# Performance work log

Measured on AMD Instinct MI355X. Metric: run time of the kernel, lower is better.

## Reference

```python
import jax, jax.numpy as jnp
import numpy as np

EMBED = 1024
ATTN = 1024
HEADS = 16
HEAD_DIM = ATTN // HEADS


def setup_inputs() -> dict:
    key = jax.random.key(0)
    ks = jax.random.split(key, 8)
    s = 1.0 / np.sqrt(EMBED)
    sa = 1.0 / np.sqrt(ATTN)
    return {
        "queries": jax.random.normal(ks[0], (4, 512, EMBED), jnp.float32),
        "context": jax.random.normal(ks[1], (4, 2048, EMBED), jnp.float32),
        "Wq": jax.random.normal(ks[2], (EMBED, ATTN), jnp.float32) * s,
        "bq": jnp.zeros((ATTN,), jnp.float32),
        "Wkv": jax.random.normal(ks[3], (EMBED, 2 * ATTN), jnp.float32) * s,
        "bkv": jnp.zeros((2 * ATTN,), jnp.float32),
        "Wo": jax.random.normal(ks[4], (ATTN, EMBED), jnp.float32) * sa,
        "bo": jnp.zeros((EMBED,), jnp.float32),
    }


def reference(queries, context, Wq, bq, Wkv, bkv, Wo, bo):
    B, Lq, _ = queries.shape
    Lk = context.shape[1]
    q = queries @ Wq + bq                      # [B, Lq, ATTN]
    kv = context @ Wkv + bkv                   # [B, Lk, 2*ATTN]
    k, v = jnp.split(kv, 2, axis=-1)
    q = q.reshape(B, Lq, HEADS, HEAD_DIM)
    k = k.reshape(B, Lk, HEADS, HEAD_DIM)
    v = v.reshape(B, Lk, HEADS, HEAD_DIM)
    scale = 1.0 / np.sqrt(HEAD_DIM)
    scores = jnp.einsum("bqhd,bkhd->bhqk", q, k) * scale
    attn = jax.nn.softmax(scores, axis=-1)
    x = jnp.einsum("bhqk,bkhd->bqhd", attn, v).reshape(B, Lq, ATTN)
    return x @ Wo + bo
```

## Files before the change

### kernel.cpp

```cpp
#include <hip/hip_runtime.h>
#include <hip/hip_bf16.h>
#include <stdint.h>

typedef unsigned short u16;
typedef __attribute__((ext_vector_type(8))) __bf16 bf16x8;
typedef __attribute__((ext_vector_type(2))) __bf16 bf16x2;
typedef __attribute__((ext_vector_type(4))) float f32x4;
typedef __attribute__((ext_vector_type(4))) u16 u16x4;
typedef __attribute__((ext_vector_type(4))) float f32x4v;

typedef __attribute__((address_space(1))) void gvoid_t;
typedef __attribute__((address_space(3))) void lvoid_t;

#define BAR()    asm volatile("s_barrier" ::: "memory")
#define WAITV0() asm volatile("s_waitcnt vmcnt(0)" ::: "memory")
#define WAITV2() asm volatile("s_waitcnt vmcnt(2)" ::: "memory")
#define WAITV4() asm volatile("s_waitcnt vmcnt(4)" ::: "memory")
#define WAITV8() asm volatile("s_waitcnt vmcnt(8)" ::: "memory")

__device__ inline u16 f2bf(float f) {
    uint32_t u = __float_as_uint(f);
    u += 0x7fff + ((u >> 16) & 1);
    return (u16)(u >> 16);
}

__device__ inline float bf2f(u16 v) {
    return __uint_as_float(((uint32_t)v) << 16);
}

__device__ inline void gll16(const void* g, void* l) {
    __builtin_amdgcn_global_load_lds((gvoid_t*)g, (lvoid_t*)l, 16, 0, 0);
}

__device__ inline f32x4 mfma16(bf16x8 a, bf16x8 b, f32x4 c) {
    return __builtin_amdgcn_mfma_f32_16x16x32_bf16(a, b, c, 0, 0, 0);
}

__device__ inline int vslot(int r) {
    int n = r >> 4;
    return ((n >> 1) << 5) + (((r >> 2) & 3) << 3) + ((n & 1) << 2) + (r & 3);
}

__global__ __launch_bounds__(256) void prep_kernel(
        const float* __restrict__ q, const float* __restrict__ c,
        const float* __restrict__ Wq, const float* __restrict__ Wkv,
        const float* __restrict__ Wo, u16* __restrict__ qb,
        u16* __restrict__ cb, u16* __restrict__ WqT,
        u16* __restrict__ WkvT, u16* __restrict__ WoT) {
    const int bid = blockIdx.x;
    const int tid = threadIdx.x;
    if (bid < 10240) {
        int i = bid * 256 + tid;
        const float* src; u16* dst; int j;
        if (i < 524288) { src = q; dst = qb; j = i; }
        else            { src = c; dst = cb; j = i - 524288; }
        f32x4v f = ((const f32x4v*)src)[j];
        u16x4 o;
        o[0] = f2bf(f[0]); o[1] = f2bf(f[1]); o[2] = f2bf(f[2]); o[3] = f2bf(f[3]);
        ((u16x4*)dst)[j] = o;
        return;
    }
    int b2 = bid - 10240;
    const float* W; u16* WT; int N, n0, k0;
    if (b2 < 1024)      { W = Wq;  WT = WqT;  N = 1024; n0 = (b2 & 31) * 32; k0 = (b2 >> 5) * 32; }
    else if (b2 < 3072) { int b3 = b2 - 1024; W = Wkv; WT = WkvT; N = 2048; n0 = (b3 & 63) * 32; k0 = (b3 >> 6) * 32; }
    else                { int b3 = b2 - 3072; W = Wo;  WT = WoT;  N = 1024; n0 = (b3 & 31) * 32; k0 = (b3 >> 5) * 32; }
    __shared__ float t[32][33];
    int x = tid & 31, y = tid >> 5;
    for (int yy = y; yy < 32; yy += 8)
        t[yy][x] = W[(size_t)(k0 + yy) * N + n0 + x];
    __syncthreads();
    for (int yy = y; yy < 32; yy += 8)
        WT[(size_t)(n0 + yy) * 1024 + k0 + x] = f2bf(t[x][yy]);
}

template <int MODE>
__global__ __launch_bounds__(512, 2) void gemm_bt(
        const u16* __restrict__ A, const u16* __restrict__ Bt,
        const float* __restrict__ bias, int M, int N, int K,
        float scale, void* __restrict__ out0) {
    __shared__ u16 lds[4][6144];
    const int NT = K >> 5;
    const int tid = threadIdx.x;
    const int lane = tid & 63, wv = tid >> 6;
    const int c16 = lane & 15, g = lane >> 4;
    const int m0 = blockIdx.y * 64, n0 = blockIdx.x * 128;

    const int idxA = (wv & 3) * 64 + lane;
    const int rA = idxA >> 2, ccA = (idxA & 3) ^ ((rA >> 1) & 3);
    const size_t offA = (size_t)(m0 + rA) * K + ccA * 8;
    const int dstA = (wv & 3) * 512;
    const int idxB = wv * 64 + lane;
    const int rB = idxB >> 2, ccB = (idxB & 3) ^ ((rB >> 1) & 3);
    const size_t offB = (size_t)(n0 + rB) * K + ccB * 8;
    const int dstB = 2048 + wv * 512;

    auto stage = [&](int t) {
        gll16(A + offA + t * 32, &lds[t & 3][dstA]);
        gll16(Bt + offB + t * 32, &lds[t & 3][dstB]);
    };

    const int wm = (wv >> 1) * 16, wn = (wv & 1) * 64;
    f32x4 acc[4] = {};

    auto compute = [&](int slot) {
        const u16* la = &lds[slot][0];
        const u16* lb = &lds[slot][2048];
        int rowa = wm + c16;
        bf16x8 af = *(const bf16x8*)&la[rowa * 32 + (g ^ ((rowa >> 1) & 3)) * 8];
        bf16x8 bfr[4];
#pragma unroll
        for (int n = 0; n < 4; n++) {
            int row = wn + n * 16 + c16;
            bfr[n] = *(const bf16x8*)&lb[row * 32 + (g ^ ((row >> 1) & 3)) * 8];
        }
#pragma unroll
        for (int n = 0; n < 4; n++)
            acc[n] = mfma16(af, bfr[n], acc[n]);
    };

    stage(0); stage(1); stage(2);

    for (int t = 0; t < NT - 2; ++t) {
        WAITV4();
        BAR();
        if (t + 3 < NT) stage(t + 3);
        compute(t & 3);
    }
    WAITV2(); BAR(); compute((NT - 2) & 3);
    WAITV0(); BAR(); compute((NT - 1) & 3);

#pragma unroll
    for (int n = 0; n < 4; n++) {
        int col = n0 + wn + n * 16 + c16;
        float bv = bias[col];
        int rowb = m0 + wm + g * 4;
#pragma unroll
        for (int j = 0; j < 4; j++) {
            float v = (acc[n][j] + bv) * scale;
            int row = rowb + j;
            if (MODE == 0) {
                ((u16*)out0)[(size_t)row * N + col] = f2bf(v);
            } else {
                ((float*)out0)[(size_t)row * N + col] = v;
            }
        }
    }
}

__global__ __launch_bounds__(512, 2) void gemm_kv_ring(
        const u16* __restrict__ A, const u16* __restrict__ Bt,
        const float* __restrict__ bias, u16* __restrict__ Kp,
        u16* __restrict__ VpT) {
    __shared__ u16 lds[4][2][256 * 32];
    const int K = 1024, NT = 32;
    const int tid = threadIdx.x;
    const int lane = tid & 63, wv = tid >> 6;
    const int c16 = lane & 15, g = lane >> 4;

    const int nwg = gridDim.x * gridDim.y;
    const int bid = blockIdx.y * gridDim.x + blockIdx.x;
    const int cpx = nwg >> 3;
    const int sw = (bid & 7) * cpx + (bid >> 3);
    const int bx = sw % gridDim.x, by = sw / gridDim.x;
    const int m0 = by * 256, n0 = bx * 256;

    const int isB = wv >> 2;
    const int rbase = (wv & 3) * 64;
    const u16* src = isB ? Bt : A;
    const int base0 = isB ? n0 : m0;
    size_t off[4];
    const u16* ldst[4];
#pragma unroll
    for (int i = 0; i < 4; i++) {
        int rl = rbase + i * 16 + (lane >> 2);
        int ch = (lane & 3) ^ ((rl >> 1) & 3);
        off[i] = (size_t)(base0 + rl) * K + ch * 8;
        ldst[i] = &lds[0][0][0] + ((size_t)isB * 256 * 32) + (size_t)(rbase + i * 16) * 32;
    }
    const size_t slotStride = 2 * 256 * 32;

    auto stage = [&](int t) {
        const u16* s0 = src + (size_t)t * 32;
        u16* d = (u16*)ldst[0] + (size_t)(t & 3) * slotStride;
        gll16(s0 + off[0], d);
        gll16(s0 + off[1], d + 16 * 32);
        gll16(s0 + off[2], d + 32 * 32);
        gll16(s0 + off[3], d + 48 * 32);
    };

    const int wm = wv >> 2;
    const int wn = wv & 3;
    f32x4 acc[8][4] = {};

    auto compute = [&](int slot) {
        const u16* la = &lds[slot][0][0];
        const u16* lb = &lds[slot][1][0];
        bf16x8 af[8], bfr[4];
#pragma unroll
        for (int m = 0; m < 8; m++) {
            int row = wm * 128 + m * 16 + c16;
            af[m] = *(const bf16x8*)&la[row * 32 + (g ^ ((row >> 1) & 3)) * 8];
        }
#pragma unroll
        for (int n = 0; n < 4; n++) {
            int row = wn * 64 + n * 16 + c16;
            bfr[n] = *(const bf16x8*)&lb[row * 32 + (g ^ ((row >> 1) & 3)) * 8];
        }
#pragma unroll
        for (int m = 0; m < 8; m++)
#pragma unroll
            for (int n = 0; n < 4; n++)
                acc[m][n] = mfma16(af[m], bfr[n], acc[m][n]);
    };

    stage(0); stage(1); stage(2);

    for (int t = 0; t < NT - 2; ++t) {
        WAITV8();
        BAR();
        if (t + 3 < NT) stage(t + 3);
        compute(t & 3);
    }
    WAITV4(); BAR(); compute((NT - 2) & 3);
    WAITV0(); BAR(); compute((NT - 1) & 3);

    const bool isV = (n0 >= 1024);
#pragma unroll
    for (int n = 0; n < 4; n++) {
        int col = n0 + wn * 64 + n * 16 + c16;
        float bv = bias[col];
#pragma unroll
        for (int m = 0; m < 8; m++) {
            int rowb = m0 + wm * 128 + m * 16 + g * 4;
            if (isV) {
                u16x4 pk;
#pragma unroll
                for (int j = 0; j < 4; j++) pk[j] = f2bf(acc[m][n][j] + bv);
                int vcol = (rowb & ~63) + vslot(rowb & 63);
                *(u16x4*)&VpT[(size_t)(col - 1024) * 8192 + vcol] = pk;
            } else {
#pragma unroll
                for (int j = 0; j < 4; j++)
                    Kp[(size_t)(rowb + j) * 1024 + col] = f2bf(acc[m][n][j] + bv);
            }
        }
    }
}

__global__ __launch_bounds__(256, 3) void attn_split_kernel(
        const u16* __restrict__ Qp, const u16* __restrict__ Kp,
        const u16* __restrict__ VpT, u16* __restrict__ Opart,
        float* __restrict__ ml) {
    __shared__ u16 lKV[3][2][64 * 64];
    const int NT = 8;
    const int tid = threadIdx.x;
    const int lane = tid & 63, wv = tid >> 6;
    const int c16 = lane & 15, g = lane >> 4;
    const int bid = blockIdx.x;
    const int qblk = bid >> 8;
    const int low = bid & 255;
    const int h = low & 15, z = low >> 4;
    const int b = z >> 2, sp = z & 3;
    const int kvbase = sp * 512;

    bf16x8 qf[2][2];
#pragma unroll
    for (int qs = 0; qs < 2; qs++) {
        int qrow = b * 512 + qblk * 128 + qs * 64 + wv * 16 + c16;
        qf[qs][0] = *(const bf16x8*)(Qp + (size_t)qrow * 1024 + h * 64 + g * 8);
        qf[qs][1] = *(const bf16x8*)(Qp + (size_t)qrow * 1024 + h * 64 + 32 + g * 8);
    }

    f32x4 acc[2][4] = {};
    float m_s[2] = {-1e30f, -1e30f}, l_s[2] = {0.f, 0.f};

    const int r0 = tid >> 3, c0 = (tid & 7) ^ (r0 & 7);
    const int r1 = 32 + r0,  c1 = (tid & 7) ^ (r1 & 7);
    const int dst0 = wv * 512, dst1 = 2048 + wv * 512;

    auto stageKV = [&](int t) {
        int slot = t % 3;
        int kv0 = kvbase + t * 64;
        u16* dK = &lKV[slot][0][0];
        u16* dV = &lKV[slot][1][0];
        gll16(Kp + (size_t)(b * 2048 + kv0 + r0) * 1024 + h * 64 + c0 * 8, dK + dst0);
        gll16(Kp + (size_t)(b * 2048 + kv0 + r1) * 1024 + h * 64 + c1 * 8, dK + dst1);
        gll16(VpT + (size_t)(h * 64 + r0) * 8192 + b * 2048 + kv0 + c0 * 8, dV + dst0);
        gll16(VpT + (size_t)(h * 64 + r1) * 8192 + b * 2048 + kv0 + c1 * 8, dV + dst1);
    };

    stageKV(0); stageKV(1);
    for (int t = 0; t < NT; ++t) {
        if (t < NT - 1) { WAITV4(); } else { WAITV0(); }
        BAR();
        if (t + 2 < NT) stageKV(t + 2);

        const int slot = t % 3;
        const u16* lK = &lKV[slot][0][0];
        const u16* lV = &lKV[slot][1][0];

        f32x4 s[2][4];
#pragma unroll
        for (int n = 0; n < 4; n++) {
            s[0][n] = f32x4{0.f, 0.f, 0.f, 0.f};
            s[1][n] = f32x4{0.f, 0.f, 0.f, 0.f};
        }
#pragma unroll
        for (int n = 0; n < 4; n++) {
            int key = n * 16 + c16;
#pragma unroll
            for (int kk = 0; kk < 2; kk++) {
                bf16x8 kf = *(const bf16x8*)&lK[key * 64 + (((kk * 4 + g) ^ (key & 7))) * 8];
                s[0][n] = mfma16(kf, qf[0][kk], s[0][n]);
                s[1][n] = mfma16(kf, qf[1][kk], s[1][n]);
            }
        }

        uint32_t r[2][4][2];
#pragma unroll
        for (int qs = 0; qs < 2; qs++) {
            float mn0 = fmaxf(fmaxf(s[qs][0][0], s[qs][0][1]), fmaxf(s[qs][0][2], s[qs][0][3]));
            float mn1 = fmaxf(fmaxf(s[qs][1][0], s[qs][1][1]), fmaxf(s[qs][1][2], s[qs][1][3]));
            float mn2 = fmaxf(fmaxf(s[qs][2][0], s[qs][2][1]), fmaxf(s[qs][2][2], s[qs][2][3]));
            float mn3 = fmaxf(fmaxf(s[qs][3][0], s[qs][3][1]), fmaxf(s[qs][3][2], s[qs][3][3]));
            float mx = fmaxf(fmaxf(mn0, mn1), fmaxf(mn2, mn3));
            mx = fmaxf(mx, __shfl_xor(mx, 16));
            mx = fmaxf(mx, __shfl_xor(mx, 32));

            if (!__all(mx - m_s[qs] <= 8.0f)) {
                float mn = fmaxf(m_s[qs], mx);
                float al = exp2f(m_s[qs] - mn);
                m_s[qs] = mn;
                l_s[qs] *= al;
                float alr[4];
#pragma unroll
                for (int j = 0; j < 4; j++) alr[j] = __shfl(al, g * 4 + j);
#pragma unroll
                for (int nd = 0; nd < 4; nd++)
#pragma unroll
                    for (int j = 0; j < 4; j++) acc[qs][nd][j] *= alr[j];
            }

            float sums[4];
#pragma unroll
            for (int n = 0; n < 4; n++) {
                float p0 = exp2f(s[qs][n][0] - m_s[qs]);
                float p1 = exp2f(s[qs][n][1] - m_s[qs]);
                float p2 = exp2f(s[qs][n][2] - m_s[qs]);
                float p3 = exp2f(s[qs][n][3] - m_s[qs]);
                sums[n] = (p0 + p1) + (p2 + p3);
                union { bf16x2 h; uint32_t u; } ca, cb;
                ca.h[0] = (__bf16)p0; ca.h[1] = (__bf16)p1;
                cb.h[0] = (__bf16)p2; cb.h[1] = (__bf16)p3;
                r[qs][n][0] = ca.u; r[qs][n][1] = cb.u;
            }
            float sum = (sums[0] + sums[1]) + (sums[2] + sums[3]);
            sum += __shfl_xor(sum, 16);
            sum += __shfl_xor(sum, 32);
            l_s[qs] += sum;
        }

#pragma unroll
        for (int kk2 = 0; kk2 < 2; kk2++) {
            union { bf16x8 v8; uint32_t u[4]; } pa0, pa1;
            pa0.u[0] = r[0][kk2 * 2][0];     pa0.u[1] = r[0][kk2 * 2][1];
            pa0.u[2] = r[0][kk2 * 2 + 1][0]; pa0.u[3] = r[0][kk2 * 2 + 1][1];
            pa1.u[0] = r[1][kk2 * 2][0];     pa1.u[1] = r[1][kk2 * 2][1];
            pa1.u[2] = r[1][kk2 * 2 + 1][0]; pa1.u[3] = r[1][kk2 * 2 + 1][1];
#pragma unroll
            for (int nd = 0; nd < 4; nd++) {
                int d = nd * 16 + c16;
                bf16x8 vf = *(const bf16x8*)&lV[d * 64 + (((kk2 * 4 + g) ^ (d & 7))) * 8];
                acc[0][nd] = mfma16(pa0.v8, vf, acc[0][nd]);
                acc[1][nd] = mfma16(pa1.v8, vf, acc[1][nd]);
            }
        }
    }

#pragma unroll
    for (int qs = 0; qs < 2; qs++) {
#pragma unroll
        for (int j = 0; j < 4; j++) {
            int rowq = b * 512 + qblk * 128 + qs * 64 + wv * 16 + g * 4 + j;
            size_t idx = (size_t)sp * 32768 + (size_t)rowq * 16 + h;
#pragma unroll
            for (int nd = 0; nd < 4; nd++)
                Opart[idx * 64 + nd * 16 + c16] = f2bf(acc[qs][nd][j]);
        }
        if (g == 0) {
            int rowq = b * 512 + qblk * 128 + qs * 64 + wv * 16 + c16;
            size_t idx = (size_t)sp * 32768 + (size_t)rowq * 16 + h;
            ml[idx * 2] = m_s[qs];
            ml[idx * 2 + 1] = l_s[qs];
        }
    }
}

__global__ __launch_bounds__(256) void attn_combine_kernel(
        const u16* __restrict__ Opart, const float* __restrict__ ml,
        u16* __restrict__ X) {
    const int tid = threadIdx.x;
    const int r = blockIdx.x * 4 + (tid >> 6);
    const int d = tid & 63;
    float m[4], l[4];
#pragma unroll
    for (int i = 0; i < 4; i++) {
        m[i] = ml[((size_t)i * 32768 + r) * 2];
        l[i] = ml[((size_t)i * 32768 + r) * 2 + 1];
    }
    float M = fmaxf(fmaxf(m[0], m[1]), fmaxf(m[2], m[3]));
    float den = 0.f, num = 0.f;
#pragma unroll
    for (int i = 0; i < 4; i++) {
        float a = exp2f(m[i] - M);
        den += l[i] * a;
        num += bf2f(Opart[((size_t)i * 32768 + r) * 64 + d]) * a;
    }
    float o = num / den;
    int qrow = r >> 4, h = r & 15;
    X[(size_t)qrow * 1024 + h * 64 + d] = f2bf(o);
}

extern "C" void kernel_launch(void* const* d_in, const int* in_sizes, int n_in,
                              void* d_out, int out_size, void* d_ws, size_t ws_size,
                              hipStream_t stream) {
    const float* queries = (const float*)d_in[0];
    const float* context = (const float*)d_in[1];
    const float* Wq      = (const float*)d_in[2];
    const float* bq      = (const float*)d_in[3];
    const float* Wkv     = (const float*)d_in[4];
    const float* bkv     = (const float*)d_in[5];
    const float* Wo      = (const float*)d_in[6];
    const float* bo      = (const float*)d_in[7];

    char* ws = (char*)d_ws;
    u16* qb   = (u16*)(ws);
    u16* cb   = (u16*)(ws + (4ull  << 20));
    u16* WqT  = (u16*)(ws + (20ull << 20));
    u16* WkvT = (u16*)(ws + (22ull << 20));
    u16* WoT  = (u16*)(ws + (26ull << 20));
    u16* Qp   = (u16*)(ws + (28ull << 20));
    u16* Kp   = (u16*)(ws + (32ull << 20));
    u16* VpT  = (u16*)(ws + (48ull << 20));
    u16* X    = (u16*)(ws + (64ull << 20));
    float* ml    = (float*)qb;
    u16*   Opart = (u16*)cb;

    prep_kernel<<<dim3(14336), dim3(256), 0, stream>>>(queries, context, Wq, Wkv, Wo,
                                                       qb, cb, WqT, WkvT, WoT);

    gemm_bt<0><<<dim3(8, 32), dim3(512), 0, stream>>>(qb, WqT, bq, 2048, 1024, 1024,
                                                      0.18033688f, (void*)Qp);
    gemm_kv_ring<<<dim3(8, 32), dim3(512), 0, stream>>>(cb, WkvT, bkv, Kp, VpT);
    attn_split_kernel<<<dim3(1024), dim3(256), 0, stream>>>(Qp, Kp, VpT, Opart, ml);
    attn_combine_kernel<<<dim3(8192), dim3(256), 0, stream>>>(Opart, ml, X);
    gemm_bt<2><<<dim3(8, 32), dim3(512), 0, stream>>>(X, WoT, bo, 2048, 1024, 1024,
                                                      1.0f, d_out);
}
```

Baseline: 120.1 us.

## Shrink KV GEMM tile to 256x128 with 3-stage ring; halve attention KV splits

The KV projection GEMM now uses a 256x128 tile and a 3-slot LDS ring instead of 256x256 with 4 slots. The grid doubles to 512 workgroups, and LDS use and accumulator registers per block drop. The split-KV attention goes from 4 splits to 2, each covering 1024 keys, and the combine kernel is rewritten for two partials. Together these aim to improve occupancy and wave count on the GEMM and to cut partial-output traffic and combine work, at the cost of lower per-tile reuse and fewer attention blocks (512).

Result: slower. 126.3 us (+5.1%).

```diff
diff --git a/kernel.cpp b/kernel.cpp
--- a/kernel.cpp
+++ b/kernel.cpp
@@ -15,8 +15,8 @@
 #define BAR()    asm volatile("s_barrier" ::: "memory")
 #define WAITV0() asm volatile("s_waitcnt vmcnt(0)" ::: "memory")
 #define WAITV2() asm volatile("s_waitcnt vmcnt(2)" ::: "memory")
+#define WAITV3() asm volatile("s_waitcnt vmcnt(3)" ::: "memory")
 #define WAITV4() asm volatile("s_waitcnt vmcnt(4)" ::: "memory")
-#define WAITV8() asm volatile("s_waitcnt vmcnt(8)" ::: "memory")
 
 __device__ inline u16 f2bf(float f) {
     uint32_t u = __float_as_uint(f);
@@ -152,7 +152,7 @@
         const u16* __restrict__ A, const u16* __restrict__ Bt,
         const float* __restrict__ bias, u16* __restrict__ Kp,
         u16* __restrict__ VpT) {
-    __shared__ u16 lds[4][2][256 * 32];
+    __shared__ u16 lds[3][12288];
     const int K = 1024, NT = 32;
     const int tid = threadIdx.x;
     const int lane = tid & 63, wv = tid >> 6;
@@ -163,43 +163,34 @@
     const int cpx = nwg >> 3;
     const int sw = (bid & 7) * cpx + (bid >> 3);
     const int bx = sw % gridDim.x, by = sw / gridDim.x;
-    const int m0 = by * 256, n0 = bx * 256;
-
-    const int isB = wv >> 2;
-    const int rbase = (wv & 3) * 64;
-    const u16* src = isB ? Bt : A;
-    const int base0 = isB ? n0 : m0;
-    size_t off[4];
-    const u16* ldst[4];
-#pragma unroll
-    for (int i = 0; i < 4; i++) {
-        int rl = rbase + i * 16 + (lane >> 2);
-        int ch = (lane & 3) ^ ((rl >> 1) & 3);
-        off[i] = (size_t)(base0 + rl) * K + ch * 8;
-        ldst[i] = &lds[0][0][0] + ((size_t)isB * 256 * 32) + (size_t)(rbase + i * 16) * 32;
-    }
-    const size_t slotStride = 2 * 256 * 32;
+    const int m0 = by * 256, n0 = bx * 128;
+
+    const int iA0 = tid,        rA0 = iA0 >> 2, cA0 = (iA0 & 3) ^ ((rA0 >> 1) & 3);
+    const int iA1 = tid + 512,  rA1 = iA1 >> 2, cA1 = (iA1 & 3) ^ ((rA1 >> 1) & 3);
+    const size_t offA0 = (size_t)(m0 + rA0) * K + cA0 * 8;
+    const size_t offA1 = (size_t)(m0 + rA1) * K + cA1 * 8;
+    const int rB = tid >> 2, cB = (tid & 3) ^ ((rB >> 1) & 3);
+    const size_t offB = (size_t)(n0 + rB) * K + cB * 8;
+    const int dstA0 = wv * 512, dstA1 = 4096 + wv * 512, dstB = 8192 + wv * 512;
 
     auto stage = [&](int t) {
-        const u16* s0 = src + (size_t)t * 32;
-        u16* d = (u16*)ldst[0] + (size_t)(t & 3) * slotStride;
-        gll16(s0 + off[0], d);
-        gll16(s0 + off[1], d + 16 * 32);
-        gll16(s0 + off[2], d + 32 * 32);
-        gll16(s0 + off[3], d + 48 * 32);
+        u16* d = &lds[t % 3][0];
+        gll16(A + offA0 + t * 32, d + dstA0);
+        gll16(A + offA1 + t * 32, d + dstA1);
+        gll16(Bt + offB + t * 32, d + dstB);
     };
 
-    const int wm = wv >> 2;
-    const int wn = wv & 3;
-    f32x4 acc[8][4] = {};
+    const int wm = wv >> 1;
+    const int wn = wv & 1;
+    f32x4 acc[4][4] = {};
 
     auto compute = [&](int slot) {
-        const u16* la = &lds[slot][0][0];
-        const u16* lb = &lds[slot][1][0];
-        bf16x8 af[8], bfr[4];
-#pragma unroll
-        for (int m = 0; m < 8; m++) {
-            int row = wm * 128 + m * 16 + c16;
+        const u16* la = &lds[slot][0];
+        const u16* lb = &lds[slot][8192];
+        bf16x8 af[4], bfr[4];
+#pragma unroll
+        for (int m = 0; m < 4; m++) {
+            int row = wm * 64 + m * 16 + c16;
             af[m] = *(const bf16x8*)&la[row * 32 + (g ^ ((row >> 1) & 3)) * 8];
         }
 #pragma unroll
@@ -208,22 +199,20 @@
             bfr[n] = *(const bf16x8*)&lb[row * 32 + (g ^ ((row >> 1) & 3)) * 8];
         }
 #pragma unroll
-        for (int m = 0; m < 8; m++)
+        for (int m = 0; m < 4; m++)
 #pragma unroll
             for (int n = 0; n < 4; n++)
                 acc[m][n] = mfma16(af[m], bfr[n], acc[m][n]);
     };
 
-    stage(0); stage(1); stage(2);
-
-    for (int t = 0; t < NT - 2; ++t) {
-        WAITV8();
+    stage(0); stage(1);
+
+    for (int t = 0; t < NT; ++t) {
+        if (t < NT - 1) { WAITV3(); } else { WAITV0(); }
         BAR();
-        if (t + 3 < NT) stage(t + 3);
-        compute(t & 3);
-    }
-    WAITV4(); BAR(); compute((NT - 2) & 3);
-    WAITV0(); BAR(); compute((NT - 1) & 3);
+        if (t + 2 < NT) stage(t + 2);
+        compute(t % 3);
+    }
 
     const bool isV = (n0 >= 1024);
 #pragma unroll
@@ -231,8 +220,8 @@
         int col = n0 + wn * 64 + n * 16 + c16;
         float bv = bias[col];
 #pragma unroll
-        for (int m = 0; m < 8; m++) {
-            int rowb = m0 + wm * 128 + m * 16 + g * 4;
+        for (int m = 0; m < 4; m++) {
+            int rowb = m0 + wm * 64 + m * 16 + g * 4;
             if (isV) {
                 u16x4 pk;
 #pragma unroll
@@ -253,16 +242,16 @@
         const u16* __restrict__ VpT, u16* __restrict__ Opart,
         float* __restrict__ ml) {
     __shared__ u16 lKV[3][2][64 * 64];
-    const int NT = 8;
+    const int NT = 16;
     const int tid = threadIdx.x;
     const int lane = tid & 63, wv = tid >> 6;
     const int c16 = lane & 15, g = lane >> 4;
     const int bid = blockIdx.x;
-    const int qblk = bid >> 8;
-    const int low = bid & 255;
+    const int qblk = bid >> 7;
+    const int low = bid & 127;
     const int h = low & 15, z = low >> 4;
-    const int b = z >> 2, sp = z & 3;
-    const int kvbase = sp * 512;
+    const int b = z >> 1, sp = z & 1;
+    const int kvbase = sp * 1024;
 
     bf16x8 qf[2][2];
 #pragma unroll
@@ -403,21 +392,14 @@
     const int tid = threadIdx.x;
     const int r = blockIdx.x * 4 + (tid >> 6);
     const int d = tid & 63;
-    float m[4], l[4];
-#pragma unroll
-    for (int i = 0; i < 4; i++) {
-        m[i] = ml[((size_t)i * 32768 + r) * 2];
-        l[i] = ml[((size_t)i * 32768 + r) * 2 + 1];
-    }
-    float M = fmaxf(fmaxf(m[0], m[1]), fmaxf(m[2], m[3]));
-    float den = 0.f, num = 0.f;
-#pragma unroll
-    for (int i = 0; i < 4; i++) {
-        float a = exp2f(m[i] - M);
-        den += l[i] * a;
-        num += bf2f(Opart[((size_t)i * 32768 + r) * 64 + d]) * a;
-    }
-    float o = num / den;
+    float m0 = ml[(size_t)r * 2], l0 = ml[(size_t)r * 2 + 1];
+    float m1 = ml[(size_t)(32768 + r) * 2], l1 = ml[(size_t)(32768 + r) * 2 + 1];
+    float M = fmaxf(m0, m1);
+    float a0 = exp2f(m0 - M), a1 = exp2f(m1 - M);
+    float li = 1.f / (l0 * a0 + l1 * a1);
+    float o0 = bf2f(Opart[(size_t)r * 64 + d]);
+    float o1 = bf2f(Opart[(size_t)(32768 + r) * 64 + d]);
+    float o = (o0 * a0 + o1 * a1) * li;
     int qrow = r >> 4, h = r & 15;
     X[(size_t)qrow * 1024 + h * 64 + d] = f2bf(o);
 }
@@ -452,8 +434,8 @@
 
     gemm_bt<0><<<dim3(8, 32), dim3(512), 0, stream>>>(qb, WqT, bq, 2048, 1024, 1024,
                                                       0.18033688f, (void*)Qp);
-    gemm_kv_ring<<<dim3(8, 32), dim3(512), 0, stream>>>(cb, WkvT, bkv, Kp, VpT);
-    attn_split_kernel<<<dim3(1024), dim3(256), 0, stream>>>(Qp, Kp, VpT, Opart, ml);
+    gemm_kv_ring<<<dim3(16, 32), dim3(512), 0, stream>>>(cb, WkvT, bkv, Kp, VpT);
+    attn_split_kernel<<<dim3(512), dim3(256), 0, stream>>>(Qp, Kp, VpT, Opart, ml);
     attn_combine_kernel<<<dim3(8192), dim3(256), 0, stream>>>(Opart, ml, X);
     gemm_bt<2><<<dim3(8, 32), dim3(512), 0, stream>>>(X, WoT, bo, 2048, 1024, 1024,
                                                       1.0f, d_out);
```

## Fuse Q and KV projection GEMMs into one launch; add MFMA priority hints

Applied to the files above, without the earlier changes.

Merges the Q projection GEMM and the KV projection GEMM into a single kernel whose grid runs 256 large KV tiles and 256 smaller Q tiles side by side. This removes one launch and lets the two independent GEMMs share the GPU instead of running back to back, which fills the tail of the KV GEMM. The attention kernel also raises wave priority around its MFMA blocks with s_setprio. The cost is load imbalance, since Q tiles are much smaller than KV tiles, and a larger register footprint from the combined kernel body.

After: 116.7 us. 2.8% less time.

```diff
diff --git a/kernel.cpp b/kernel.cpp
--- a/kernel.cpp
+++ b/kernel.cpp
@@ -148,101 +148,166 @@
     }
 }
 
-__global__ __launch_bounds__(512, 2) void gemm_kv_ring(
-        const u16* __restrict__ A, const u16* __restrict__ Bt,
-        const float* __restrict__ bias, u16* __restrict__ Kp,
-        u16* __restrict__ VpT) {
-    __shared__ u16 lds[4][2][256 * 32];
-    const int K = 1024, NT = 32;
+__global__ __launch_bounds__(512, 2) void fused_qkv(
+        const u16* __restrict__ cb, const u16* __restrict__ WkvT,
+        const float* __restrict__ bkv, u16* __restrict__ Kp,
+        u16* __restrict__ VpT,
+        const u16* __restrict__ qb, const u16* __restrict__ WqT,
+        const float* __restrict__ bq, float qscale, u16* __restrict__ Qp) {
+    __shared__ u16 smem[4][2][8192];
     const int tid = threadIdx.x;
     const int lane = tid & 63, wv = tid >> 6;
     const int c16 = lane & 15, g = lane >> 4;
-
-    const int nwg = gridDim.x * gridDim.y;
-    const int bid = blockIdx.y * gridDim.x + blockIdx.x;
-    const int cpx = nwg >> 3;
-    const int sw = (bid & 7) * cpx + (bid >> 3);
-    const int bx = sw % gridDim.x, by = sw / gridDim.x;
-    const int m0 = by * 256, n0 = bx * 256;
-
-    const int isB = wv >> 2;
-    const int rbase = (wv & 3) * 64;
-    const u16* src = isB ? Bt : A;
-    const int base0 = isB ? n0 : m0;
-    size_t off[4];
-    const u16* ldst[4];
-#pragma unroll
-    for (int i = 0; i < 4; i++) {
-        int rl = rbase + i * 16 + (lane >> 2);
-        int ch = (lane & 3) ^ ((rl >> 1) & 3);
-        off[i] = (size_t)(base0 + rl) * K + ch * 8;
-        ldst[i] = &lds[0][0][0] + ((size_t)isB * 256 * 32) + (size_t)(rbase + i * 16) * 32;
-    }
-    const size_t slotStride = 2 * 256 * 32;
-
-    auto stage = [&](int t) {
-        const u16* s0 = src + (size_t)t * 32;
-        u16* d = (u16*)ldst[0] + (size_t)(t & 3) * slotStride;
-        gll16(s0 + off[0], d);
-        gll16(s0 + off[1], d + 16 * 32);
-        gll16(s0 + off[2], d + 32 * 32);
-        gll16(s0 + off[3], d + 48 * 32);
-    };
-
-    const int wm = wv >> 2;
-    const int wn = wv & 3;
-    f32x4 acc[8][4] = {};
-
-    auto compute = [&](int slot) {
-        const u16* la = &lds[slot][0][0];
-        const u16* lb = &lds[slot][1][0];
-        bf16x8 af[8], bfr[4];
-#pragma unroll
-        for (int m = 0; m < 8; m++) {
-            int row = wm * 128 + m * 16 + c16;
-            af[m] = *(const bf16x8*)&la[row * 32 + (g ^ ((row >> 1) & 3)) * 8];
-        }
+    const int bidg = blockIdx.x;
+
+    if (bidg < 256) {
+        const int K = 1024, NT = 32;
+        const int cpx = 32;
+        const int sw = (bidg & 7) * cpx + (bidg >> 3);
+        const int bx = sw & 7, by = sw >> 3;
+        const int m0 = by * 256, n0 = bx * 256;
+
+        const int isB = wv >> 2;
+        const int rbase = (wv & 3) * 64;
+        const u16* src = isB ? WkvT : cb;
+        const int base0 = isB ? n0 : m0;
+        size_t off[4];
+        const u16* ldst[4];
+#pragma unroll
+        for (int i = 0; i < 4; i++) {
+            int rl = rbase + i * 16 + (lane >> 2);
+            int ch = (lane & 3) ^ ((rl >> 1) & 3);
+            off[i] = (size_t)(base0 + rl) * K + ch * 8;
+            ldst[i] = &smem[0][0][0] + ((size_t)isB * 256 * 32) + (size_t)(rbase + i * 16) * 32;
+        }
+        const size_t slotStride = 2 * 256 * 32;
+
+        auto stage = [&](int t) {
+            const u16* s0 = src + (size_t)t * 32;
+            u16* d = (u16*)ldst[0] + (size_t)(t & 3) * slotStride;
+            gll16(s0 + off[0], d);
+            gll16(s0 + off[1], d + 16 * 32);
+            gll16(s0 + off[2], d + 32 * 32);
+            gll16(s0 + off[3], d + 48 * 32);
+        };
+
+        const int wm = wv >> 2;
+        const int wn = wv & 3;
+        f32x4 acc[8][4] = {};
+
+        auto compute = [&](int slot) {
+            const u16* la = &smem[slot][0][0];
+            const u16* lb = &smem[slot][1][0];
+            bf16x8 af[8], bfr[4];
+#pragma unroll
+            for (int m = 0; m < 8; m++) {
+                int row = wm * 128 + m * 16 + c16;
+                af[m] = *(const bf16x8*)&la[row * 32 + (g ^ ((row >> 1) & 3)) * 8];
+            }
+#pragma unroll
+            for (int n = 0; n < 4; n++) {
+                int row = wn * 64 + n * 16 + c16;
+                bfr[n] = *(const bf16x8*)&lb[row * 32 + (g ^ ((row >> 1) & 3)) * 8];
+            }
+#pragma unroll
+            for (int m = 0; m < 8; m++)
+#pragma unroll
+                for (int n = 0; n < 4; n++)
+                    acc[m][n] = mfma16(af[m], bfr[n], acc[m][n]);
+        };
+
+        stage(0); stage(1); stage(2);
+
+        for (int t = 0; t < NT - 2; ++t) {
+            WAITV8();
+            BAR();
+            if (t + 3 < NT) stage(t + 3);
+            compute(t & 3);
+        }
+        WAITV4(); BAR(); compute((NT - 2) & 3);
+        WAITV0(); BAR(); compute((NT - 1) & 3);
+
+        const bool isV = (n0 >= 1024);
 #pragma unroll
         for (int n = 0; n < 4; n++) {
-            int row = wn * 64 + n * 16 + c16;
-            bfr[n] = *(const bf16x8*)&lb[row * 32 + (g ^ ((row >> 1) & 3)) * 8];
-        }
-#pragma unroll
-        for (int m = 0; m < 8; m++)
+            int col = n0 + wn * 64 + n * 16 + c16;
+            float bv = bkv[col];
+#pragma unroll
+            for (int m = 0; m < 8; m++) {
+                int rowb = m0 + wm * 128 + m * 16 + g * 4;
+                if (isV) {
+                    u16x4 pk;
+#pragma unroll
+                    for (int j = 0; j < 4; j++) pk[j] = f2bf(acc[m][n][j] + bv);
+                    int vcol = (rowb & ~63) + vslot(rowb & 63);
+                    *(u16x4*)&VpT[(size_t)(col - 1024) * 8192 + vcol] = pk;
+                } else {
+#pragma unroll
+                    for (int j = 0; j < 4; j++)
+                        Kp[(size_t)(rowb + j) * 1024 + col] = f2bf(acc[m][n][j] + bv);
+                }
+            }
+        }
+    } else {
+        const int K = 1024, N = 1024, NT = 32;
+        const int b2 = bidg - 256;
+        const int m0 = (b2 >> 3) * 64, n0 = (b2 & 7) * 128;
+        u16* base = &smem[0][0][0];
+
+        const int idxA = (wv & 3) * 64 + lane;
+        const int rA = idxA >> 2, ccA = (idxA & 3) ^ ((rA >> 1) & 3);
+        const size_t offA = (size_t)(m0 + rA) * K + ccA * 8;
+        const int dstA = (wv & 3) * 512;
+        const int idxB = wv * 64 + lane;
+        const int rB = idxB >> 2, ccB = (idxB & 3) ^ ((rB >> 1) & 3);
+        const size_t offB = (size_t)(n0 + rB) * K + ccB * 8;
+        const int dstB = 2048 + wv * 512;
+
+        auto stage = [&](int t) {
+            u16* d = base + (t & 3) * 6144;
+            gll16(qb + offA + t * 32, d + dstA);
+            gll16(WqT + offB + t * 32, d + dstB);
+        };
+
+        const int wm = (wv >> 1) * 16, wn = (wv & 1) * 64;
+        f32x4 acc[4] = {};
+
+        auto compute = [&](int slot) {
+            const u16* la = base + slot * 6144;
+            const u16* lb = la + 2048;
+            int rowa = wm + c16;
+            bf16x8 af = *(const bf16x8*)&la[rowa * 32 + (g ^ ((rowa >> 1) & 3)) * 8];
+            bf16x8 bfr[4];
+#pragma unroll
+            for (int n = 0; n < 4; n++) {
+                int row = wn + n * 16 + c16;
+                bfr[n] = *(const bf16x8*)&lb[row * 32 + (g ^ ((row >> 1) & 3)) * 8];
+            }
 #pragma unroll
             for (int n = 0; n < 4; n++)
-                acc[m][n] = mfma16(af[m], bfr[n], acc[m][n]);
-    };
-
-    stage(0); stage(1); stage(2);
-
-    for (int t = 0; t < NT - 2; ++t) {
-        WAITV8();
-        BAR();
-        if (t + 3 < NT) stage(t + 3);
-        compute(t & 3);
-    }
-    WAITV4(); BAR(); compute((NT - 2) & 3);
-    WAITV0(); BAR(); compute((NT - 1) & 3);
-
-    const bool isV = (n0 >= 1024);
-#pragma unroll
-    for (int n = 0; n < 4; n++) {
-        int col = n0 + wn * 64 + n * 16 + c16;
-        float bv = bias[col];
-#pragma unroll
-        for (int m = 0; m < 8; m++) {
-            int rowb = m0 + wm * 128 + m * 16 + g * 4;
-            if (isV) {
-                u16x4 pk;
-#pragma unroll
-                for (int j = 0; j < 4; j++) pk[j] = f2bf(acc[m][n][j] + bv);
-                int vcol = (rowb & ~63) + vslot(rowb & 63);
-                *(u16x4*)&VpT[(size_t)(col - 1024) * 8192 + vcol] = pk;
-            } else {
-#pragma unroll
-                for (int j = 0; j < 4; j++)
-                    Kp[(size_t)(rowb + j) * 1024 + col] = f2bf(acc[m][n][j] + bv);
+                acc[n] = mfma16(af, bfr[n], acc[n]);
+        };
+
+        stage(0); stage(1); stage(2);
+
+        for (int t = 0; t < NT - 2; ++t) {
+            WAITV4();
+            BAR();
+            if (t + 3 < NT) stage(t + 3);
+            compute(t & 3);
+        }
+        WAITV2(); BAR(); compute((NT - 2) & 3);
+        WAITV0(); BAR(); compute((NT - 1) & 3);
+
+#pragma unroll
+        for (int n = 0; n < 4; n++) {
+            int col = n0 + wn + n * 16 + c16;
+            float bv = bq[col];
+            int rowb = m0 + wm + g * 4;
+#pragma unroll
+            for (int j = 0; j < 4; j++) {
+                float v = (acc[n][j] + bv) * qscale;
+                Qp[(size_t)(rowb + j) * N + col] = f2bf(v);
             }
         }
     }
@@ -306,6 +371,7 @@
             s[0][n] = f32x4{0.f, 0.f, 0.f, 0.f};
             s[1][n] = f32x4{0.f, 0.f, 0.f, 0.f};
         }
+        __builtin_amdgcn_s_setprio(1);
 #pragma unroll
         for (int n = 0; n < 4; n++) {
             int key = n * 16 + c16;
@@ -316,6 +382,7 @@
                 s[1][n] = mfma16(kf, qf[1][kk], s[1][n]);
             }
         }
+        __builtin_amdgcn_s_setprio(0);
 
         uint32_t r[2][4][2];
 #pragma unroll
@@ -361,6 +428,7 @@
             l_s[qs] += sum;
         }
 
+        __builtin_amdgcn_s_setprio(1);
 #pragma unroll
         for (int kk2 = 0; kk2 < 2; kk2++) {
             union { bf16x8 v8; uint32_t u[4]; } pa0, pa1;
@@ -376,6 +444,7 @@
                 acc[1][nd] = mfma16(pa1.v8, vf, acc[1][nd]);
             }
         }
+        __builtin_amdgcn_s_setprio(0);
     }
 
 #pragma unroll
@@ -450,9 +519,8 @@
     prep_kernel<<<dim3(14336), dim3(256), 0, stream>>>(queries, context, Wq, Wkv, Wo,
                                                        qb, cb, WqT, WkvT, WoT);
 
-    gemm_bt<0><<<dim3(8, 32), dim3(512), 0, stream>>>(qb, WqT, bq, 2048, 1024, 1024,
-                                                      0.18033688f, (void*)Qp);
-    gemm_kv_ring<<<dim3(8, 32), dim3(512), 0, stream>>>(cb, WkvT, bkv, Kp, VpT);
+    fused_qkv<<<dim3(512), dim3(512), 0, stream>>>(cb, WkvT, bkv, Kp, VpT,
+                                                   qb, WqT, bq, 0.18033688f, Qp);
     attn_split_kernel<<<dim3(1024), dim3(256), 0, stream>>>(Qp, Kp, VpT, Opart, ml);
     attn_combine_kernel<<<dim3(8192), dim3(256), 0, stream>>>(Opart, ml, X);
     gemm_bt<2><<<dim3(8, 32), dim3(512), 0, stream>>>(X, WoT, bo, 2048, 1024, 1024,
```
